# Performance work log

Hardware: AMD Instinct MI355X
Metric: run time of the kernel (lower is better)

Reference implementation:

```python
import jax, jax.numpy as jnp
import numpy as np
import math

B, L, D, A, VD, H = 8, 2048, 1024, 1024, 1024, 1024
EPS = 1e-5

def gelu(x):
    return 0.5 * x * (1.0 + jax.lax.erf(x / math.sqrt(2.0)))

def setup_inputs() -> dict:
    key = jax.random.key(0)
    ks = jax.random.split(key, 12)
    s = 0.02
    return {
        "Q": jax.random.normal(ks[0], (B, L, D), jnp.float32),
        "K": jax.random.normal(ks[1], (B, L, D), jnp.float32),
        "V": jax.random.normal(ks[2], (B, L, D), jnp.float32),
        "attn_mask": jax.random.randint(ks[3], (B, L, L), 0, 2, jnp.int32),
        "Wq": jax.random.normal(ks[4], (D, A), jnp.float32) * s,
        "bq": jnp.zeros((A,), jnp.float32),
        "Wk": jax.random.normal(ks[5], (D, A), jnp.float32) * s,
        "bk": jnp.zeros((A,), jnp.float32),
        "Wv": jax.random.normal(ks[6], (D, VD), jnp.float32) * s,
        "bv": jnp.zeros((VD,), jnp.float32),
        "Wo": jax.random.normal(ks[7], (VD, H), jnp.float32) * s,
        "bo": jnp.zeros((H,), jnp.float32),
        "gamma": jnp.ones((H,), jnp.float32),
        "beta": jnp.zeros((H,), jnp.float32),
    }

def reference(Q, K, V, attn_mask, Wq, bq, Wk, bk, Wv, bv, Wo, bo, gamma, beta):
    q = Q @ Wq + bq                      # [B,L,A]
    k = K @ Wk + bk                      # [B,L,A]
    scores = jnp.einsum('bqa,bka->bqk', q, k) / math.sqrt(A)
    scores = scores + attn_mask.astype(jnp.float32) * (-1e9)
    scores = jnp.swapaxes(scores, -1, -2)  # [B,Lk,Lq]; softmax over QUERY axis
    attn = jax.nn.softmax(scores, axis=-1)
    wv = V @ Wv + bv                     # [B,L,VD]
    context = jnp.einsum('bkq,bqv->bkv', attn, wv)  # [B,L,VD]
    context = gelu(context @ Wo + bo)    # [B,L,H]
    mu = jnp.mean(context, axis=-1, keepdims=True)
    var = jnp.var(context, axis=-1, keepdims=True)
    context = (context - mu) / jnp.sqrt(var + EPS) * gamma + beta
    return context, attn
```

## Files before the change

### kernel.cpp

```cpp
#include <hip/hip_runtime.h>
#include <math.h>

typedef __bf16 bf16;
typedef __bf16 bf16x8 __attribute__((ext_vector_type(8)));
typedef __bf16 bf16x4 __attribute__((ext_vector_type(4)));
typedef float f32x4 __attribute__((ext_vector_type(4)));
typedef signed char schar8 __attribute__((ext_vector_type(8)));

__device__ inline void gload16(const void* g, void* l) {
  typedef __attribute__((address_space(1))) const unsigned int guint;
  typedef __attribute__((address_space(3))) unsigned int luint;
  __builtin_amdgcn_global_load_lds((guint*)g, (luint*)l, 16, 0, 0);
}

template<int BIAS_MODE, bool MASK, bool GELU, bool OUT_BF16>
__global__ __launch_bounds__(512, 2)
void bgemm8_k(const bf16* __restrict__ A, const bf16* __restrict__ B,
              const float* __restrict__ bias, const float* __restrict__ bias2,
              const signed char* __restrict__ mT,
              void* __restrict__ Cout, int N, int ldc, int K,
              long sAb, long sBb, long sCb, long sMb, float scale)
{
  __shared__ __align__(16) char smem[131072];
  bf16* As = (bf16*)smem;
  bf16* Bs = (bf16*)(smem + 65536);

  const int t    = threadIdx.x;
  const int zb   = blockIdx.z;
  const int gx   = gridDim.x;
  const int nwg  = gx * gridDim.y;
  const int orig = blockIdx.y * gx + blockIdx.x;
  const int swz  = (orig & 7) * (nwg >> 3) + (orig >> 3);
  const int m0   = (swz / gx) * 256;
  const int n0   = (swz % gx) * 256;

  const float* bp = (BIAS_MODE && bias2 && zb) ? bias2 : bias;

  const int wave = t >> 6;
  const int lane = t & 63;
  const int wm = wave >> 2;
  const int wn = wave & 3;
  const int fr = lane & 15;
  const int fg = lane >> 4;

  const bf16* Abase = A + (size_t)zb * sAb + (size_t)m0 * K;
  const bf16* Bbase = B + (size_t)zb * sBb + (size_t)n0 * K;
  size_t gOff[2];
  int    ldsOff[2];
#pragma unroll
  for (int j = 0; j < 2; ++j) {
    const int L   = j * 8192 + t * 16;
    const int row = L >> 6;
    const int gp  = (L >> 4) & 3;
    const int g   = gp ^ ((row >> 1) & 3);
    gOff[j]   = (size_t)row * K + (size_t)g * 8;
    ldsOff[j] = j * 4096 + wave * 512;
  }
  const int HMAX = (K >> 5) * 2;

  auto stage = [&](int H) {
    if (H >= HMAX) return;
    const int s    = H >> 1;
    const int slot = s & 3;
    const size_t kof = (size_t)s * 32;
    if ((H & 1) == 0) {
      gload16(Abase + kof + gOff[0], As + slot * 8192 + ldsOff[0]);
      gload16(Abase + kof + gOff[1], As + slot * 8192 + ldsOff[1]);
    } else {
      gload16(Bbase + kof + gOff[0], Bs + slot * 8192 + ldsOff[0]);
      gload16(Bbase + kof + gOff[1], Bs + slot * 8192 + ldsOff[1]);
    }
  };

  const int xsw  = (fg ^ ((fr >> 1) & 3)) * 8;
  const int aoff = (wm * 128 + fr) * 32 + xsw;
  const int boff = (wn * 64 + fr) * 32 + xsw;

  f32x4 acc[8][4] = {};
  const int T = K >> 6;

  stage(0); stage(1); stage(2); stage(3); stage(4);
  asm volatile("s_waitcnt vmcnt(6)" ::: "memory");
  __builtin_amdgcn_s_barrier();

  for (int tt = 0; tt < T; ++tt) {
#pragma unroll
    for (int p = 0; p < 4; ++p) {
      const int kk   = p & 1;
      const int oh   = p >> 1;
      const int slot = (2 * tt + kk) & 3;
      bf16x8 af[4], bfv[4];
#pragma unroll
      for (int i = 0; i < 4; ++i)
        af[i]  = *(const bf16x8*)(As + slot * 8192 + aoff + (oh * 4 + i) * 512);
#pragma unroll
      for (int i = 0; i < 4; ++i)
        bfv[i] = *(const bf16x8*)(Bs + slot * 8192 + boff + i * 512);
      stage(4 * tt + p + 5);
      __builtin_amdgcn_s_barrier();
      __builtin_amdgcn_s_setprio(1);
#pragma unroll
      for (int mi = 0; mi < 4; ++mi)
#pragma unroll
        for (int ni = 0; ni < 4; ++ni)
          acc[oh * 4 + mi][ni] =
            __builtin_amdgcn_mfma_f32_16x16x32_bf16(af[mi], bfv[ni], acc[oh * 4 + mi][ni], 0, 0, 0);
      __builtin_amdgcn_s_setprio(0);
      if (p == 0) {
        if (tt == T - 1) asm volatile("s_waitcnt vmcnt(0)" ::: "memory");
        else             asm volatile("s_waitcnt vmcnt(4)" ::: "memory");
      }
      if (p == 3) {
        if (tt < T - 2)       asm volatile("s_waitcnt vmcnt(6)" ::: "memory");
        else if (tt == T - 2) asm volatile("s_waitcnt vmcnt(4)" ::: "memory");
      }
      __builtin_amdgcn_s_barrier();
    }
  }

  if constexpr (OUT_BF16) {
    bf16* wbuf = (bf16*)(smem + wave * 16384);
#pragma unroll
    for (int mi = 0; mi < 8; ++mi) {
#pragma unroll
      for (int ni = 0; ni < 4; ++ni) {
        const int col = n0 + wn * 64 + ni * 16 + fr;
#pragma unroll
        for (int i = 0; i < 4; ++i) {
          const int r = mi * 16 + fg * 4 + i;
          float v = acc[mi][ni][i] * scale;
          if constexpr (BIAS_MODE == 1) v += bp[col];
          if constexpr (BIAS_MODE == 2) v += bp[m0 + wm * 128 + r];
          if constexpr (GELU) v = 0.5f * v * (1.0f + erff(v * 0.70710678118f));
          const int cb = ni * 32 + fr * 2;
          *(bf16*)((char*)wbuf + r * 128 + (cb ^ ((r & 7) << 4))) = (bf16)v;
        }
      }
    }
    __syncthreads();
    const int rowbase = m0 + wm * 128;
    const int colbase = n0 + wn * 64;
    const signed char* mb = MASK ? (mT + (size_t)zb * sMb) : nullptr;
#pragma unroll
    for (int j = 0; j < 16; ++j) {
      const int r  = j * 8 + (lane >> 3);
      const int cg = lane & 7;
      bf16x8 val = *(const bf16x8*)((char*)wbuf + r * 128 + ((cg << 4) ^ ((r & 7) << 4)));
      const int grow = rowbase + r;
      const int gcol = colbase + cg * 8;
      if constexpr (MASK) {
        schar8 mk = *(const schar8*)(mb + (size_t)grow * N + gcol);
#pragma unroll
        for (int e = 0; e < 8; ++e)
          val[e] = (bf16)((float)val[e] + -1e9f * (float)mk[e]);
      }
      *(bf16x8*)((bf16*)Cout + (size_t)zb * sCb + (size_t)grow * ldc + gcol) = val;
    }
  } else {
#pragma unroll
    for (int mi = 0; mi < 8; ++mi) {
#pragma unroll
      for (int ni = 0; ni < 4; ++ni) {
        const int col = n0 + wn * 64 + ni * 16 + fr;
#pragma unroll
        for (int i = 0; i < 4; ++i) {
          const int r = m0 + wm * 128 + mi * 16 + fg * 4 + i;
          float v = acc[mi][ni][i] * scale;
          if constexpr (BIAS_MODE == 1) v += bp[col];
          if constexpr (BIAS_MODE == 2) v += bp[r];
          if constexpr (GELU) v = 0.5f * v * (1.0f + erff(v * 0.70710678118f));
          ((float*)Cout)[(size_t)zb * sCb + (size_t)r * ldc + col] = v;
        }
      }
    }
  }
}

__global__ __launch_bounds__(256)
void conv2_k(const float* __restrict__ i0, const float* __restrict__ i1,
             bf16* __restrict__ o0, bf16* __restrict__ o1, long n8)
{
  const float* in = blockIdx.z ? i1 : i0;
  bf16* out = blockIdx.z ? o1 : o0;
  for (long i = blockIdx.x * 256 + threadIdx.x; i < n8; i += (long)gridDim.x * 256) {
    f32x4 a = *(const f32x4*)(in + i * 8);
    f32x4 b = *(const f32x4*)(in + i * 8 + 4);
    bf16x8 o;
#pragma unroll
    for (int j = 0; j < 4; ++j) { o[j] = (bf16)a[j]; o[4 + j] = (bf16)b[j]; }
    *(bf16x8*)(out + i * 8) = o;
  }
}

__global__ __launch_bounds__(256)
void wtrans_k(const float* __restrict__ W0, const float* __restrict__ W1,
              const float* __restrict__ W2, const float* __restrict__ W3,
              bf16* __restrict__ out)
{
  const float* Ws[4] = {W0, W1, W2, W3};
  const float* W = Ws[blockIdx.z];
  bf16* o = out + (size_t)blockIdx.z * (1024 * 1024);
  __shared__ bf16 tile[64][72];
  const int t  = threadIdx.x;
  const int c0 = blockIdx.x * 64;
  const int r0 = blockIdx.y * 64;
  {
    const int rr = t >> 2;
    const int cc = (t & 3) * 16;
    const float* src = W + (size_t)(r0 + rr) * 1024 + c0 + cc;
#pragma unroll
    for (int j = 0; j < 16; j += 4) {
      f32x4 v = *(const f32x4*)(src + j);
#pragma unroll
      for (int i = 0; i < 4; ++i) tile[cc + j + i][rr] = (bf16)v[i];
    }
  }
  __syncthreads();
  {
    const int nr = t >> 2;
    const int kc = (t & 3) * 16;
    bf16* dst = o + (size_t)(c0 + nr) * 1024 + r0 + kc;
    *(bf16x8*)dst       = *(const bf16x8*)&tile[nr][kc];
    *(bf16x8*)(dst + 8) = *(const bf16x8*)&tile[nr][kc + 8];
  }
}

__global__ __launch_bounds__(256)
void maskT_k(const int* __restrict__ mask, signed char* __restrict__ mT)
{
  __shared__ signed char tile[64][65];
  const int t  = threadIdx.x;
  const int b  = blockIdx.z;
  const int k0 = blockIdx.x * 64;
  const int q0 = blockIdx.y * 64;
  {
    const int iq = t >> 2;
    const int ic = (t & 3) * 16;
    const int* src = mask + ((size_t)b * 2048 + q0 + iq) * 2048 + k0 + ic;
#pragma unroll
    for (int j = 0; j < 16; j += 4) {
      int4 v = *(const int4*)(src + j);
      tile[ic + j + 0][iq] = (signed char)v.x;
      tile[ic + j + 1][iq] = (signed char)v.y;
      tile[ic + j + 2][iq] = (signed char)v.z;
      tile[ic + j + 3][iq] = (signed char)v.w;
    }
  }
  __syncthreads();
  {
    const int ik = t >> 2;
    const int iq = (t & 3) * 16;
    signed char* dst = mT + ((size_t)b * 2048 + k0 + ik) * 2048 + q0 + iq;
#pragma unroll
    for (int j = 0; j < 16; ++j) dst[j] = tile[ik][iq + j];
  }
}

__global__ __launch_bounds__(256)
void softmax_rows_k(float* __restrict__ P, bf16* __restrict__ Pb)
{
  char* slot = (char*)P + (size_t)blockIdx.x * 8192;
  const bf16* pin = (const bf16*)slot;
  float* pout = (float*)slot;
  bf16* pb = Pb + (size_t)blockIdx.x * 2048;
  const int t = threadIdx.x;
  const int wave = t >> 6, lane = t & 63;
  bf16x8 raw = *(const bf16x8*)(pin + t * 8);
  float v[8];
#pragma unroll
  for (int j = 0; j < 8; ++j) v[j] = (float)raw[j];
  float m = -3e38f;
#pragma unroll
  for (int j = 0; j < 8; ++j) m = fmaxf(m, v[j]);
#pragma unroll
  for (int off = 32; off; off >>= 1) m = fmaxf(m, __shfl_xor(m, off));
  __shared__ float red[8];
  if (lane == 0) red[wave] = m;
  __syncthreads();
  m = fmaxf(fmaxf(red[0], red[1]), fmaxf(red[2], red[3]));
  float s = 0.0f;
#pragma unroll
  for (int j = 0; j < 8; ++j) { v[j] = __expf(v[j] - m); s += v[j]; }
#pragma unroll
  for (int off = 32; off; off >>= 1) s += __shfl_xor(s, off);
  if (lane == 0) red[4 + wave] = s;
  __syncthreads();
  s = red[4] + red[5] + red[6] + red[7];
  const float inv = 1.0f / s;
  f32x4 o0, o1;
  bf16x8 ob;
#pragma unroll
  for (int j = 0; j < 4; ++j) {
    o0[j] = v[j] * inv; o1[j] = v[4 + j] * inv;
    ob[j] = (bf16)o0[j]; ob[4 + j] = (bf16)o1[j];
  }
  *(f32x4*)(pout + t * 8)     = o0;
  *(f32x4*)(pout + t * 8 + 4) = o1;
  *(bf16x8*)(pb + t * 8)      = ob;
}

__global__ __launch_bounds__(256)
void ln_k(const bf16* __restrict__ g, const float* __restrict__ gamma,
          const float* __restrict__ beta, float* __restrict__ out)
{
  const bf16* p = g + (size_t)blockIdx.x * 1024;
  const int t = threadIdx.x;
  const int wave = t >> 6, lane = t & 63;
  bf16x4 raw = *(const bf16x4*)(p + t * 4);
  f32x4 v;
#pragma unroll
  for (int j = 0; j < 4; ++j) v[j] = (float)raw[j];
  float s = v[0] + v[1] + v[2] + v[3];
  float q = v[0]*v[0] + v[1]*v[1] + v[2]*v[2] + v[3]*v[3];
#pragma unroll
  for (int off = 32; off; off >>= 1) { s += __shfl_xor(s, off); q += __shfl_xor(q, off); }
  __shared__ float red[16];
  if (lane == 0) { red[wave] = s; red[8 + wave] = q; }
  __syncthreads();
  s = red[0] + red[1] + red[2] + red[3];
  q = red[8] + red[9] + red[10] + red[11];
  const float mu   = s * (1.0f / 1024.0f);
  const float var  = q * (1.0f / 1024.0f) - mu * mu;
  const float rstd = rsqrtf(var + 1e-5f);
  f32x4 gm = *(const f32x4*)(gamma + t * 4);
  f32x4 bt = *(const f32x4*)(beta + t * 4);
  f32x4 o;
#pragma unroll
  for (int j = 0; j < 4; ++j) o[j] = (v[j] - mu) * rstd * gm[j] + bt[j];
  *(f32x4*)(out + (size_t)blockIdx.x * 1024 + t * 4) = o;
}

extern "C" void kernel_launch(void* const* d_in, const int* in_sizes, int n_in,
                              void* d_out, int out_size, void* d_ws, size_t ws_size,
                              hipStream_t stream)
{
  const float* Q     = (const float*)d_in[0];
  const float* Kin   = (const float*)d_in[1];
  const float* V     = (const float*)d_in[2];
  const int*   mask  = (const int*)d_in[3];
  const float* Wq    = (const float*)d_in[4];
  const float* bq    = (const float*)d_in[5];
  const float* Wk    = (const float*)d_in[6];
  const float* bk    = (const float*)d_in[7];
  const float* Wv    = (const float*)d_in[8];
  const float* bv    = (const float*)d_in[9];
  const float* Wo    = (const float*)d_in[10];
  const float* bo    = (const float*)d_in[11];
  const float* gamma = (const float*)d_in[12];
  const float* beta  = (const float*)d_in[13];

  float* outCtx  = (float*)d_out;
  float* outAttn = outCtx + (size_t)8 * 2048 * 1024;

  char* ws = (char*)d_ws;
  const size_t MB = 1048576;
  bf16*        wts   = (bf16*)(ws + 0 * MB);
  bf16*        qp    = (bf16*)(ws + 8 * MB);
  bf16*        kp    = (bf16*)(ws + 40 * MB);
  bf16*        Qb    = (bf16*)(ws + 72 * MB);
  bf16*        Kb    = (bf16*)(ws + 104 * MB);
  signed char* mT    = (signed char*)(ws + 72 * MB);
  bf16*        attnb = (bf16*)(ws + 40 * MB);
  bf16*        wvT   = (bf16*)(ws + 8 * MB);
  bf16*        Vb    = (bf16*)(ws + 104 * MB);
  bf16*        ctx   = (bf16*)(ws + 104 * MB);
  bf16*        g     = (bf16*)(ws + 40 * MB);
  bf16* Wqt = wts;
  bf16* Wkt = wts + 1 * 1024 * 1024;
  bf16* Wvt = wts + 2 * 1024 * 1024;
  bf16* Wot = wts + 3 * 1024 * 1024;

  const dim3 blk(256);
  const dim3 blk8(512);
  const long n8 = (long)16384 * 1024 / 8;

  wtrans_k<<<dim3(16, 16, 4), blk, 0, stream>>>(Wq, Wk, Wv, Wo, wts);
  conv2_k<<<dim3(2048, 1, 2), blk, 0, stream>>>(Q, Kin, Qb, Kb, n8);
  bgemm8_k<1, false, false, true><<<dim3(4, 64, 2), blk8, 0, stream>>>(
      Qb, Wqt, bq, bk, nullptr, qp, 1024, 1024, 1024,
      16777216, 1048576, 16777216, 0, 1.0f);
  conv2_k<<<dim3(2048, 1, 1), blk, 0, stream>>>(V, nullptr, Vb, nullptr, n8);
  maskT_k<<<dim3(32, 32, 8), blk, 0, stream>>>(mask, mT);
  bgemm8_k<0, true, false, true><<<dim3(8, 8, 8), blk8, 0, stream>>>(
      kp, qp, nullptr, nullptr, mT, (bf16*)outAttn, 2048, 4096, 1024,
      (long)2048 * 1024, (long)2048 * 1024, (long)2048 * 4096, (long)2048 * 2048, 0.03125f);
  bgemm8_k<2, false, false, true><<<dim3(8, 4, 8), blk8, 0, stream>>>(
      Wvt, Vb, bv, nullptr, nullptr, wvT, 2048, 2048, 1024,
      0, (long)2048 * 1024, (long)1024 * 2048, 0, 1.0f);
  softmax_rows_k<<<dim3(16384), blk, 0, stream>>>(outAttn, attnb);
  bgemm8_k<0, false, false, true><<<dim3(4, 8, 8), blk8, 0, stream>>>(
      attnb, wvT, nullptr, nullptr, nullptr, ctx, 1024, 1024, 2048,
      (long)2048 * 2048, (long)1024 * 2048, (long)2048 * 1024, 0, 1.0f);
  bgemm8_k<1, false, true, true><<<dim3(4, 64, 1), blk8, 0, stream>>>(
      ctx, Wot, bo, nullptr, nullptr, g, 1024, 1024, 1024, 0, 0, 0, 0, 1.0f);
  ln_k<<<dim3(16384), blk, 0, stream>>>(g, gamma, beta, outCtx);
}
```

Before: 489.6 us.

## Merge preprocessing kernels, move mask add into softmax, use XCD-aware tile mapping

Merges the weight transpose with the Q/K conversion, and the mask transpose with the V conversion, into two multi-role kernels so there are fewer launches. Moves the -1e9 mask addition out of the score GEMM epilogue into the softmax, which now reads the transposed mask row directly. Replaces the generic block swizzle with a per-launch parameterized mapping (cx, rx, ry) meant to keep neighbouring tiles on the same XCD for L2 reuse. Splits the bf16 attention buffer across two workspace regions, selected by batch index in the PV GEMM. The main risk is the new aliasing of workspace regions between stages.

Result: no change. 491.3 us (+0.3%).

```diff
diff --git a/kernel.cpp b/kernel.cpp
--- a/kernel.cpp
+++ b/kernel.cpp
@@ -13,13 +13,14 @@
   __builtin_amdgcn_global_load_lds((guint*)g, (luint*)l, 16, 0, 0);
 }
 
-template<int BIAS_MODE, bool MASK, bool GELU, bool OUT_BF16>
+template<int BIAS_MODE, bool GELU>
 __global__ __launch_bounds__(512, 2)
-void bgemm8_k(const bf16* __restrict__ A, const bf16* __restrict__ B,
+void bgemm8_k(const bf16* __restrict__ A, const bf16* __restrict__ A2,
+              const bf16* __restrict__ B,
               const float* __restrict__ bias, const float* __restrict__ bias2,
-              const signed char* __restrict__ mT,
-              void* __restrict__ Cout, int N, int ldc, int K,
-              long sAb, long sBb, long sCb, long sMb, float scale)
+              bf16* __restrict__ Cout, int ldc, int K,
+              long sAb, long sBb, long sCb, float scale,
+              int cx, int rx, int ry)
 {
   __shared__ __align__(16) char smem[131072];
   bf16* As = (bf16*)smem;
@@ -27,12 +28,13 @@
 
   const int t    = threadIdx.x;
   const int zb   = blockIdx.z;
-  const int gx   = gridDim.x;
-  const int nwg  = gx * gridDim.y;
-  const int orig = blockIdx.y * gx + blockIdx.x;
-  const int swz  = (orig & 7) * (nwg >> 3) + (orig >> 3);
-  const int m0   = (swz / gx) * 256;
-  const int n0   = (swz % gx) * 256;
+  const int lin  = blockIdx.y * gridDim.x + blockIdx.x;
+  const int c    = lin & 7;
+  const int s    = lin >> 3;
+  const int n_tile = (c % cx) * rx + (s % rx);
+  const int m_tile = (c / cx) * ry + (s / rx);
+  const int m0   = m_tile << 8;
+  const int n0   = n_tile << 8;
 
   const float* bp = (BIAS_MODE && bias2 && zb) ? bias2 : bias;
 
@@ -43,7 +45,9 @@
   const int fr = lane & 15;
   const int fg = lane >> 4;
 
-  const bf16* Abase = A + (size_t)zb * sAb + (size_t)m0 * K;
+  const bf16* Aroot = (A2 && zb >= 4) ? A2 : A;
+  const int   za    = (A2 && zb >= 4) ? zb - 4 : zb;
+  const bf16* Abase = Aroot + (size_t)za * sAb + (size_t)m0 * K;
   const bf16* Bbase = B + (size_t)zb * sBb + (size_t)n0 * K;
   size_t gOff[2];
   int    ldsOff[2];
@@ -60,9 +64,9 @@
 
   auto stage = [&](int H) {
     if (H >= HMAX) return;
-    const int s    = H >> 1;
-    const int slot = s & 3;
-    const size_t kof = (size_t)s * 32;
+    const int sl   = H >> 1;
+    const int slot = sl & 3;
+    const size_t kof = (size_t)sl * 32;
     if ((H & 1) == 0) {
       gload16(Abase + kof + gOff[0], As + slot * 8192 + ldsOff[0]);
       gload16(Abase + kof + gOff[1], As + slot * 8192 + ldsOff[1]);
@@ -118,157 +122,147 @@
     }
   }
 
-  if constexpr (OUT_BF16) {
-    bf16* wbuf = (bf16*)(smem + wave * 16384);
-#pragma unroll
-    for (int mi = 0; mi < 8; ++mi) {
-#pragma unroll
-      for (int ni = 0; ni < 4; ++ni) {
-        const int col = n0 + wn * 64 + ni * 16 + fr;
-#pragma unroll
-        for (int i = 0; i < 4; ++i) {
-          const int r = mi * 16 + fg * 4 + i;
-          float v = acc[mi][ni][i] * scale;
-          if constexpr (BIAS_MODE == 1) v += bp[col];
-          if constexpr (BIAS_MODE == 2) v += bp[m0 + wm * 128 + r];
-          if constexpr (GELU) v = 0.5f * v * (1.0f + erff(v * 0.70710678118f));
-          const int cb = ni * 32 + fr * 2;
-          *(bf16*)((char*)wbuf + r * 128 + (cb ^ ((r & 7) << 4))) = (bf16)v;
-        }
+  bf16* wbuf = (bf16*)(smem + wave * 16384);
+#pragma unroll
+  for (int mi = 0; mi < 8; ++mi) {
+#pragma unroll
+    for (int ni = 0; ni < 4; ++ni) {
+      const int col = n0 + wn * 64 + ni * 16 + fr;
+#pragma unroll
+      for (int i = 0; i < 4; ++i) {
+        const int r = mi * 16 + fg * 4 + i;
+        float v = acc[mi][ni][i] * scale;
+        if constexpr (BIAS_MODE == 1) v += bp[col];
+        if constexpr (BIAS_MODE == 2) v += bp[m0 + wm * 128 + r];
+        if constexpr (GELU) v = 0.5f * v * (1.0f + erff(v * 0.70710678118f));
+        const int cb = ni * 32 + fr * 2;
+        *(bf16*)((char*)wbuf + r * 128 + (cb ^ ((r & 7) << 4))) = (bf16)v;
+      }
+    }
+  }
+  __syncthreads();
+  const int rowbase = m0 + wm * 128;
+  const int colbase = n0 + wn * 64;
+#pragma unroll
+  for (int j = 0; j < 16; ++j) {
+    const int r  = j * 8 + (lane >> 3);
+    const int cg = lane & 7;
+    bf16x8 val = *(const bf16x8*)((char*)wbuf + r * 128 + ((cg << 4) ^ ((r & 7) << 4)));
+    *(bf16x8*)(Cout + (size_t)zb * sCb + (size_t)(rowbase + r) * ldc + colbase + cg * 8) = val;
+  }
+}
+
+__global__ __launch_bounds__(256)
+void pre1_k(const float* __restrict__ W0, const float* __restrict__ W1,
+            const float* __restrict__ W2, const float* __restrict__ W3,
+            bf16* __restrict__ wts,
+            const float* __restrict__ Q, const float* __restrict__ Kin,
+            bf16* __restrict__ Qb, bf16* __restrict__ Kb, long n8)
+{
+  __shared__ __align__(16) char sb[64 * 72 * 2];
+  const int t = threadIdx.x;
+  if (blockIdx.z == 0) {
+    const float* Ws[4] = {W0, W1, W2, W3};
+    const int wsel = blockIdx.x >> 8;
+    const float* W = Ws[wsel];
+    bf16* o = wts + (size_t)wsel * (1024 * 1024);
+    const int c0 = (blockIdx.x & 15) * 64;
+    const int r0 = ((blockIdx.x >> 4) & 15) * 64;
+    bf16 (*tile)[72] = (bf16(*)[72])sb;
+    {
+      const int rr = t >> 2;
+      const int cc = (t & 3) * 16;
+      const float* src = W + (size_t)(r0 + rr) * 1024 + c0 + cc;
+#pragma unroll
+      for (int j = 0; j < 16; j += 4) {
+        f32x4 v = *(const f32x4*)(src + j);
+#pragma unroll
+        for (int i = 0; i < 4; ++i) tile[cc + j + i][rr] = (bf16)v[i];
       }
     }
     __syncthreads();
-    const int rowbase = m0 + wm * 128;
-    const int colbase = n0 + wn * 64;
-    const signed char* mb = MASK ? (mT + (size_t)zb * sMb) : nullptr;
-#pragma unroll
-    for (int j = 0; j < 16; ++j) {
-      const int r  = j * 8 + (lane >> 3);
-      const int cg = lane & 7;
-      bf16x8 val = *(const bf16x8*)((char*)wbuf + r * 128 + ((cg << 4) ^ ((r & 7) << 4)));
-      const int grow = rowbase + r;
-      const int gcol = colbase + cg * 8;
-      if constexpr (MASK) {
-        schar8 mk = *(const schar8*)(mb + (size_t)grow * N + gcol);
-#pragma unroll
-        for (int e = 0; e < 8; ++e)
-          val[e] = (bf16)((float)val[e] + -1e9f * (float)mk[e]);
-      }
-      *(bf16x8*)((bf16*)Cout + (size_t)zb * sCb + (size_t)grow * ldc + gcol) = val;
+    {
+      const int nr = t >> 2;
+      const int kc = (t & 3) * 16;
+      bf16* dst = o + (size_t)(c0 + nr) * 1024 + r0 + kc;
+      *(bf16x8*)dst       = *(const bf16x8*)&tile[nr][kc];
+      *(bf16x8*)(dst + 8) = *(const bf16x8*)&tile[nr][kc + 8];
     }
   } else {
-#pragma unroll
-    for (int mi = 0; mi < 8; ++mi) {
-#pragma unroll
-      for (int ni = 0; ni < 4; ++ni) {
-        const int col = n0 + wn * 64 + ni * 16 + fr;
-#pragma unroll
-        for (int i = 0; i < 4; ++i) {
-          const int r = m0 + wm * 128 + mi * 16 + fg * 4 + i;
-          float v = acc[mi][ni][i] * scale;
-          if constexpr (BIAS_MODE == 1) v += bp[col];
-          if constexpr (BIAS_MODE == 2) v += bp[r];
-          if constexpr (GELU) v = 0.5f * v * (1.0f + erff(v * 0.70710678118f));
-          ((float*)Cout)[(size_t)zb * sCb + (size_t)r * ldc + col] = v;
-        }
-      }
+    const float* in = (blockIdx.z == 1) ? Q : Kin;
+    bf16* out = (blockIdx.z == 1) ? Qb : Kb;
+    for (long i = blockIdx.x * 256 + t; i < n8; i += (long)gridDim.x * 256) {
+      f32x4 a = *(const f32x4*)(in + i * 8);
+      f32x4 b = *(const f32x4*)(in + i * 8 + 4);
+      bf16x8 o;
+#pragma unroll
+      for (int j = 0; j < 4; ++j) { o[j] = (bf16)a[j]; o[4 + j] = (bf16)b[j]; }
+      *(bf16x8*)(out + i * 8) = o;
     }
   }
 }
 
 __global__ __launch_bounds__(256)
-void conv2_k(const float* __restrict__ i0, const float* __restrict__ i1,
-             bf16* __restrict__ o0, bf16* __restrict__ o1, long n8)
-{
-  const float* in = blockIdx.z ? i1 : i0;
-  bf16* out = blockIdx.z ? o1 : o0;
-  for (long i = blockIdx.x * 256 + threadIdx.x; i < n8; i += (long)gridDim.x * 256) {
-    f32x4 a = *(const f32x4*)(in + i * 8);
-    f32x4 b = *(const f32x4*)(in + i * 8 + 4);
-    bf16x8 o;
-#pragma unroll
-    for (int j = 0; j < 4; ++j) { o[j] = (bf16)a[j]; o[4 + j] = (bf16)b[j]; }
-    *(bf16x8*)(out + i * 8) = o;
+void pre2_k(const int* __restrict__ mask, signed char* __restrict__ mT,
+            const float* __restrict__ V, bf16* __restrict__ Vb, long n8)
+{
+  __shared__ __align__(16) char sb[64 * 72 * 2];
+  const int t = threadIdx.x;
+  if (blockIdx.z < 8) {
+    const int b  = blockIdx.z;
+    const int k0 = (blockIdx.x & 31) * 64;
+    const int q0 = (blockIdx.x >> 5) * 64;
+    signed char (*tile)[65] = (signed char(*)[65])sb;
+    {
+      const int iq = t >> 2;
+      const int ic = (t & 3) * 16;
+      const int* src = mask + ((size_t)b * 2048 + q0 + iq) * 2048 + k0 + ic;
+#pragma unroll
+      for (int j = 0; j < 16; j += 4) {
+        int4 v = *(const int4*)(src + j);
+        tile[ic + j + 0][iq] = (signed char)v.x;
+        tile[ic + j + 1][iq] = (signed char)v.y;
+        tile[ic + j + 2][iq] = (signed char)v.z;
+        tile[ic + j + 3][iq] = (signed char)v.w;
+      }
+    }
+    __syncthreads();
+    {
+      const int ik = t >> 2;
+      const int iq = (t & 3) * 16;
+      signed char* dst = mT + ((size_t)b * 2048 + k0 + ik) * 2048 + q0 + iq;
+#pragma unroll
+      for (int j = 0; j < 16; ++j) dst[j] = tile[ik][iq + j];
+    }
+  } else {
+    for (long i = blockIdx.x * 256 + t; i < n8; i += (long)gridDim.x * 256) {
+      f32x4 a = *(const f32x4*)(V + i * 8);
+      f32x4 b = *(const f32x4*)(V + i * 8 + 4);
+      bf16x8 o;
+#pragma unroll
+      for (int j = 0; j < 4; ++j) { o[j] = (bf16)a[j]; o[4 + j] = (bf16)b[j]; }
+      *(bf16x8*)(Vb + i * 8) = o;
+    }
   }
 }
 
 __global__ __launch_bounds__(256)
-void wtrans_k(const float* __restrict__ W0, const float* __restrict__ W1,
-              const float* __restrict__ W2, const float* __restrict__ W3,
-              bf16* __restrict__ out)
-{
-  const float* Ws[4] = {W0, W1, W2, W3};
-  const float* W = Ws[blockIdx.z];
-  bf16* o = out + (size_t)blockIdx.z * (1024 * 1024);
-  __shared__ bf16 tile[64][72];
-  const int t  = threadIdx.x;
-  const int c0 = blockIdx.x * 64;
-  const int r0 = blockIdx.y * 64;
-  {
-    const int rr = t >> 2;
-    const int cc = (t & 3) * 16;
-    const float* src = W + (size_t)(r0 + rr) * 1024 + c0 + cc;
-#pragma unroll
-    for (int j = 0; j < 16; j += 4) {
-      f32x4 v = *(const f32x4*)(src + j);
-#pragma unroll
-      for (int i = 0; i < 4; ++i) tile[cc + j + i][rr] = (bf16)v[i];
-    }
-  }
-  __syncthreads();
-  {
-    const int nr = t >> 2;
-    const int kc = (t & 3) * 16;
-    bf16* dst = o + (size_t)(c0 + nr) * 1024 + r0 + kc;
-    *(bf16x8*)dst       = *(const bf16x8*)&tile[nr][kc];
-    *(bf16x8*)(dst + 8) = *(const bf16x8*)&tile[nr][kc + 8];
-  }
-}
-
-__global__ __launch_bounds__(256)
-void maskT_k(const int* __restrict__ mask, signed char* __restrict__ mT)
-{
-  __shared__ signed char tile[64][65];
-  const int t  = threadIdx.x;
-  const int b  = blockIdx.z;
-  const int k0 = blockIdx.x * 64;
-  const int q0 = blockIdx.y * 64;
-  {
-    const int iq = t >> 2;
-    const int ic = (t & 3) * 16;
-    const int* src = mask + ((size_t)b * 2048 + q0 + iq) * 2048 + k0 + ic;
-#pragma unroll
-    for (int j = 0; j < 16; j += 4) {
-      int4 v = *(const int4*)(src + j);
-      tile[ic + j + 0][iq] = (signed char)v.x;
-      tile[ic + j + 1][iq] = (signed char)v.y;
-      tile[ic + j + 2][iq] = (signed char)v.z;
-      tile[ic + j + 3][iq] = (signed char)v.w;
-    }
-  }
-  __syncthreads();
-  {
-    const int ik = t >> 2;
-    const int iq = (t & 3) * 16;
-    signed char* dst = mT + ((size_t)b * 2048 + k0 + ik) * 2048 + q0 + iq;
-#pragma unroll
-    for (int j = 0; j < 16; ++j) dst[j] = tile[ik][iq + j];
-  }
-}
-
-__global__ __launch_bounds__(256)
-void softmax_rows_k(float* __restrict__ P, bf16* __restrict__ Pb)
-{
-  char* slot = (char*)P + (size_t)blockIdx.x * 8192;
+void softmax_rows_k(float* __restrict__ P, const signed char* __restrict__ mT,
+                    bf16* __restrict__ Pb0, bf16* __restrict__ Pb1)
+{
+  const int bx = blockIdx.x;
+  char* slot = (char*)P + (size_t)bx * 8192;
   const bf16* pin = (const bf16*)slot;
   float* pout = (float*)slot;
-  bf16* pb = Pb + (size_t)blockIdx.x * 2048;
+  bf16* pb = (bx < 8192) ? (Pb0 + (size_t)bx * 2048) : (Pb1 + (size_t)(bx - 8192) * 2048);
+  const signed char* mrow = mT + (size_t)bx * 2048;
   const int t = threadIdx.x;
   const int wave = t >> 6, lane = t & 63;
   bf16x8 raw = *(const bf16x8*)(pin + t * 8);
+  schar8 mk = *(const schar8*)(mrow + t * 8);
   float v[8];
 #pragma unroll
-  for (int j = 0; j < 8; ++j) v[j] = (float)raw[j];
+  for (int j = 0; j < 8; ++j) v[j] = (float)raw[j] + (float)mk[j] * -1e9f;
   float m = -3e38f;
 #pragma unroll
   for (int j = 0; j < 8; ++j) m = fmaxf(m, v[j]);
@@ -360,13 +354,12 @@
   bf16*        Qb    = (bf16*)(ws + 72 * MB);
   bf16*        Kb    = (bf16*)(ws + 104 * MB);
   signed char* mT    = (signed char*)(ws + 72 * MB);
-  bf16*        attnb = (bf16*)(ws + 40 * MB);
+  bf16*        Vb    = (bf16*)(ws + 104 * MB);
   bf16*        wvT   = (bf16*)(ws + 8 * MB);
-  bf16*        Vb    = (bf16*)(ws + 104 * MB);
-  bf16*        ctx   = (bf16*)(ws + 104 * MB);
+  bf16*        attnb0= (bf16*)(ws + 40 * MB);
+  bf16*        attnb1= (bf16*)(ws + 104 * MB);
+  bf16*        ctx   = (bf16*)(ws + 72 * MB);
   bf16*        g     = (bf16*)(ws + 40 * MB);
-  bf16* Wqt = wts;
-  bf16* Wkt = wts + 1 * 1024 * 1024;
   bf16* Wvt = wts + 2 * 1024 * 1024;
   bf16* Wot = wts + 3 * 1024 * 1024;
 
@@ -374,24 +367,23 @@
   const dim3 blk8(512);
   const long n8 = (long)16384 * 1024 / 8;
 
-  wtrans_k<<<dim3(16, 16, 4), blk, 0, stream>>>(Wq, Wk, Wv, Wo, wts);
-  conv2_k<<<dim3(2048, 1, 2), blk, 0, stream>>>(Q, Kin, Qb, Kb, n8);
-  bgemm8_k<1, false, false, true><<<dim3(4, 64, 2), blk8, 0, stream>>>(
-      Qb, Wqt, bq, bk, nullptr, qp, 1024, 1024, 1024,
-      16777216, 1048576, 16777216, 0, 1.0f);
-  conv2_k<<<dim3(2048, 1, 1), blk, 0, stream>>>(V, nullptr, Vb, nullptr, n8);
-  maskT_k<<<dim3(32, 32, 8), blk, 0, stream>>>(mask, mT);
-  bgemm8_k<0, true, false, true><<<dim3(8, 8, 8), blk8, 0, stream>>>(
-      kp, qp, nullptr, nullptr, mT, (bf16*)outAttn, 2048, 4096, 1024,
-      (long)2048 * 1024, (long)2048 * 1024, (long)2048 * 4096, (long)2048 * 2048, 0.03125f);
-  bgemm8_k<2, false, false, true><<<dim3(8, 4, 8), blk8, 0, stream>>>(
-      Wvt, Vb, bv, nullptr, nullptr, wvT, 2048, 2048, 1024,
-      0, (long)2048 * 1024, (long)1024 * 2048, 0, 1.0f);
-  softmax_rows_k<<<dim3(16384), blk, 0, stream>>>(outAttn, attnb);
-  bgemm8_k<0, false, false, true><<<dim3(4, 8, 8), blk8, 0, stream>>>(
-      attnb, wvT, nullptr, nullptr, nullptr, ctx, 1024, 1024, 2048,
-      (long)2048 * 2048, (long)1024 * 2048, (long)2048 * 1024, 0, 1.0f);
-  bgemm8_k<1, false, true, true><<<dim3(4, 64, 1), blk8, 0, stream>>>(
-      ctx, Wot, bo, nullptr, nullptr, g, 1024, 1024, 1024, 0, 0, 0, 0, 1.0f);
+  pre1_k<<<dim3(1024, 1, 3), blk, 0, stream>>>(Wq, Wk, Wv, Wo, wts, Q, Kin, Qb, Kb, n8);
+  bgemm8_k<1, false><<<dim3(4, 64, 2), blk8, 0, stream>>>(
+      Qb, nullptr, wts, bq, bk, qp, 1024, 1024,
+      16777216, 1048576, 16777216, 1.0f, 1, 4, 8);
+  pre2_k<<<dim3(1024, 1, 9), blk, 0, stream>>>(mask, mT, V, Vb, n8);
+  bgemm8_k<0, false><<<dim3(8, 8, 8), blk8, 0, stream>>>(
+      kp, nullptr, qp, nullptr, nullptr, (bf16*)outAttn, 4096, 1024,
+      (long)2048 * 1024, (long)2048 * 1024, (long)2048 * 4096, 0.03125f, 4, 2, 4);
+  bgemm8_k<2, false><<<dim3(8, 4, 8), blk8, 0, stream>>>(
+      Wvt, nullptr, Vb, bv, nullptr, wvT, 2048, 1024,
+      0, (long)2048 * 1024, (long)1024 * 2048, 1.0f, 4, 2, 2);
+  softmax_rows_k<<<dim3(16384), blk, 0, stream>>>(outAttn, mT, attnb0, attnb1);
+  bgemm8_k<0, false><<<dim3(4, 8, 8), blk8, 0, stream>>>(
+      attnb0, attnb1, wvT, nullptr, nullptr, ctx, 1024, 2048,
+      (long)2048 * 2048, (long)1024 * 2048, (long)2048 * 1024, 1.0f, 2, 2, 2);
+  bgemm8_k<1, true><<<dim3(4, 64, 1), blk8, 0, stream>>>(
+      ctx, nullptr, Wot, bo, nullptr, g, 1024, 1024,
+      0, 0, 0, 1.0f, 1, 4, 8);
   ln_k<<<dim3(16384), blk, 0, stream>>>(g, gamma, beta, outCtx);
 }
```
